# Kernel optimization log

Measured on AMD Instinct MI355X. Metric: run time of the kernel, lower is better.

The kernel has to match this reference:

```python
import jax, jax.numpy as jnp
from jax import lax
import numpy as np

T, B, D, H = 4096, 8, 512, 512


def sru_layer(x, W, b, c0):
    # x: [T,B,D], W: [3H,D], b: [2H], c0: [B,H]
    U = jnp.einsum('tbd,hd->tbh', x, W)          # [T,B,3H] fused projection
    x_tilde, f_pre, r_pre = jnp.split(U, 3, axis=-1)
    f = jax.nn.sigmoid(f_pre + b[:H])            # forget gate [T,B,H]
    r = jax.nn.sigmoid(r_pre + b[H:])            # reset gate  [T,B,H]

    def step(c, inp):
        xt, ft = inp
        c_new = ft * c + (1.0 - ft) * xt         # elementwise recurrence
        return c_new, c_new

    c_last, cs = lax.scan(step, c0, (x_tilde, f))
    h = r * jnp.tanh(cs) + (1.0 - r) * x         # highway connection
    return h, c_last


def setup_inputs() -> dict:
    key = jax.random.key(0)
    k0, k1, k2 = jax.random.split(key, 3)
    scale = 1.0 / np.sqrt(D)
    return {
        'x': jax.random.normal(k0, (T, B, D), dtype=jnp.float32),
        'W0': jax.random.normal(k1, (3 * H, D), dtype=jnp.float32) * scale,
        'b0': jnp.zeros((2 * H,), dtype=jnp.float32),
        'W1': jax.random.normal(k2, (3 * H, H), dtype=jnp.float32) * scale,
        'b1': jnp.zeros((2 * H,), dtype=jnp.float32),
    }


def reference(x, W0, b0, W1, b1):
    c0 = jnp.zeros((x.shape[1], H), dtype=x.dtype)
    h, c = sru_layer(x, W0, b0, c0)
    h, c = sru_layer(h, W1, b1, c0)   # original resets c0 each layer
    return h, c
```

## Files before the change

### kernel.cpp

```cpp
#include <hip/hip_runtime.h>
#include <hip/hip_bf16.h>


#define T_DIM 4096
#define B_DIM 8
#define H_DIM 512
#define M_DIM (T_DIM * B_DIM)
#define N3H 1536
#define K_DIM 512
#define NCHUNK 512
#define CLEN (T_DIM / NCHUNK)
#define NCHAIN (B_DIM * H_DIM)
#define NGRP 32
#define GLEN (NCHUNK / NGRP)

typedef __attribute__((ext_vector_type(8))) short s16x8;
typedef __attribute__((ext_vector_type(4))) float f32x4;
typedef unsigned short ushort_t;
typedef unsigned int uint_t;

__device__ __forceinline__ float bf2f(ushort_t u) {
    return __uint_as_float(((uint_t)u) << 16);
}
__device__ __forceinline__ ushort_t f2bf(float f) {
    uint_t u = __float_as_uint(f);
    u += 0x7FFFu + ((u >> 16) & 1u);
    return (ushort_t)(u >> 16);
}
__device__ __forceinline__ float sigm(float z) {
    return 1.0f / (1.0f + __expf(-z));
}
__device__ __forceinline__ float tanh_fast(float z) {
    float e = __expf(2.0f * z);
    return (e - 1.0f) / (e + 1.0f);
}

#define XF4 (M_DIM * K_DIM / 4)
#define WF4 (N3H * K_DIM / 4)
__global__ void cvt_all(const float* __restrict__ x, const float* __restrict__ w0,
                        const float* __restrict__ w1, ushort_t* __restrict__ xb,
                        ushort_t* __restrict__ w0b, ushort_t* __restrict__ w1b) {
    int i = blockIdx.x * blockDim.x + threadIdx.x;
    const float* src; ushort_t* dst; int idx;
    if (i < XF4) { src = x; dst = xb; idx = i; }
    else if (i < XF4 + WF4) { src = w0; dst = w0b; idx = i - XF4; }
    else if (i < XF4 + 2 * WF4) { src = w1; dst = w1b; idx = i - XF4 - WF4; }
    else return;
    float4 v = reinterpret_cast<const float4*>(src)[idx];
    ushort4 o;
    o.x = f2bf(v.x); o.y = f2bf(v.y); o.z = f2bf(v.z); o.w = f2bf(v.w);
    reinterpret_cast<ushort4*>(dst)[idx] = o;
}

__device__ __forceinline__ s16x8 lds_swz_read(const ushort_t* base, int row, int kb) {
    int byte = (row << 7) + (((kb << 1)) ^ ((row & 7) << 4));
    return *reinterpret_cast<const s16x8*>(reinterpret_cast<const char*>(base) + byte);
}

__global__ __launch_bounds__(512) void gemm_bt256(const ushort_t* __restrict__ A,
                                                  const ushort_t* __restrict__ Bm,
                                                  ushort_t* __restrict__ C,
                                                  int M, int N, int K) {
    __shared__ ushort_t As[2][256 * 64];
    __shared__ ushort_t Bs[2][256 * 64];
    const int ntn = N >> 8;
    const int nwg = gridDim.x;
    const int bid = (int)blockIdx.x;
    const int id = (bid & 7) * (nwg >> 3) + (bid >> 3);
    const int tm = id / ntn, tn = id % ntn;
    const int row0 = tm << 8, col0 = tn << 8;
    const int tid = threadIdx.x;
    const int wv = tid >> 6, lane = tid & 63;
    const int wm = wv >> 2, wn = wv & 3;
    const int l15 = lane & 15;
    const int kgrp = (lane >> 4) << 3;

    f32x4 acc[8][4] = {};

    const int srow_in_wave = lane >> 3;
    const int sslot = lane & 7;

#define STAGE(buf_, t_)                                                                  \
    {                                                                                    \
        const int k0s = (t_) * 64;                                                       \
        _Pragma("unroll")                                                                \
        for (int j = 0; j < 4; ++j) {                                                    \
            const int rl = j * 64 + wv * 8;                                              \
            const int rme = rl + srow_in_wave;                                           \
            const int sl = sslot ^ (rme & 7);             \
            const ushort_t* ga = A + (size_t)(row0 + rme) * K + k0s + (sl << 3);         \
            const ushort_t* gb = Bm + (size_t)(col0 + rme) * K + k0s + (sl << 3);        \
            __builtin_amdgcn_global_load_lds(                                            \
                (const __attribute__((address_space(1))) void*)ga,                       \
                (__attribute__((address_space(3))) void*)&As[buf_][rl * 64], 16, 0, 0);  \
            __builtin_amdgcn_global_load_lds(                                            \
                (const __attribute__((address_space(1))) void*)gb,                       \
                (__attribute__((address_space(3))) void*)&Bs[buf_][rl * 64], 16, 0, 0);  \
        }                                                                                \
    }

    STAGE(0, 0);
    STAGE(1, 1);
    asm volatile("s_waitcnt vmcnt(8)" ::: "memory");
    __builtin_amdgcn_s_barrier();

    const int nkt = K >> 6;
    for (int t = 0; t < nkt; ++t) {
        const int buf = t & 1;
        const ushort_t* Ab = &As[buf][0];
        const ushort_t* Bb = &Bs[buf][0];

        __builtin_amdgcn_s_setprio(1);
        {
            s16x8 af[4][2], bfr[4][2];
#pragma unroll
            for (int j = 0; j < 4; ++j)
#pragma unroll
                for (int kk2 = 0; kk2 < 2; ++kk2)
                    af[j][kk2] = lds_swz_read(Ab, wm * 128 + j * 16 + l15, kk2 * 32 + kgrp);
#pragma unroll
            for (int n = 0; n < 4; ++n)
#pragma unroll
                for (int kk2 = 0; kk2 < 2; ++kk2)
                    bfr[n][kk2] = lds_swz_read(Bb, wn * 64 + n * 16 + l15, kk2 * 32 + kgrp);
#pragma unroll
            for (int j = 0; j < 4; ++j)
#pragma unroll
                for (int n = 0; n < 4; ++n)
#pragma unroll
                    for (int kk2 = 0; kk2 < 2; ++kk2)
                        acc[j][n] = __builtin_amdgcn_mfma_f32_16x16x32_bf16(af[j][kk2], bfr[n][kk2], acc[j][n], 0, 0, 0);
#pragma unroll
            for (int j = 0; j < 4; ++j)
#pragma unroll
                for (int kk2 = 0; kk2 < 2; ++kk2)
                    af[j][kk2] = lds_swz_read(Ab, wm * 128 + (4 + j) * 16 + l15, kk2 * 32 + kgrp);
#pragma unroll
            for (int j = 0; j < 4; ++j)
#pragma unroll
                for (int n = 0; n < 4; ++n)
#pragma unroll
                    for (int kk2 = 0; kk2 < 2; ++kk2)
                        acc[4 + j][n] = __builtin_amdgcn_mfma_f32_16x16x32_bf16(af[j][kk2], bfr[n][kk2], acc[4 + j][n], 0, 0, 0);
        }
        __builtin_amdgcn_s_setprio(0);
        __builtin_amdgcn_s_barrier();

        if (t + 2 < nkt) STAGE(buf, t + 2);
        if (t + 1 < nkt) {
            if (t + 2 < nkt) asm volatile("s_waitcnt vmcnt(8)" ::: "memory");
            else             asm volatile("s_waitcnt vmcnt(0)" ::: "memory");
            __builtin_amdgcn_s_barrier();
        }
    }
#undef STAGE

    const int crow = (lane >> 4) << 2;
#pragma unroll
    for (int m = 0; m < 8; ++m)
#pragma unroll
        for (int n = 0; n < 4; ++n)
#pragma unroll
            for (int v = 0; v < 4; ++v)
                C[(size_t)(row0 + wm * 128 + m * 16 + crow + v) * N + (col0 + wn * 64 + n * 16 + l15)] =
                    f2bf(acc[m][n][v]);
}

__global__ void scan_summary(const ushort_t* __restrict__ U, const float* __restrict__ bias,
                             float* __restrict__ Sa, float* __restrict__ Sb) {
    const int b = blockIdx.x / NCHUNK;
    const int chunk = blockIdx.x % NCHUNK;
    const int h = threadIdx.x << 2;
    float fb[4];
#pragma unroll
    for (int j = 0; j < 4; ++j) fb[j] = bias[h + j];
    float Aa[4] = {1.f, 1.f, 1.f, 1.f};
    float Bb[4] = {0.f, 0.f, 0.f, 0.f};
    const ushort_t* rp = U + ((size_t)(chunk * CLEN) * B_DIM + b) * N3H + h;
    ushort4 xt = *reinterpret_cast<const ushort4*>(rp);
    ushort4 fp = *reinterpret_cast<const ushort4*>(rp + H_DIM);
#pragma unroll
    for (int s = 0; s < CLEN; ++s) {
        ushort4 xt_n, fp_n;
        if (s + 1 < CLEN) {
            rp += (size_t)B_DIM * N3H;
            xt_n = *reinterpret_cast<const ushort4*>(rp);
            fp_n = *reinterpret_cast<const ushort4*>(rp + H_DIM);
        }
        float xs[4] = {bf2f(xt.x), bf2f(xt.y), bf2f(xt.z), bf2f(xt.w)};
        float fs[4] = {bf2f(fp.x), bf2f(fp.y), bf2f(fp.z), bf2f(fp.w)};
#pragma unroll
        for (int j = 0; j < 4; ++j) {
            float f = sigm(fs[j] + fb[j]);
            Aa[j] *= f;
            Bb[j] = f * Bb[j] + (1.f - f) * xs[j];
        }
        xt = xt_n; fp = fp_n;
    }
    const int cb = chunk * NCHAIN + b * H_DIM + h;
#pragma unroll
    for (int j = 0; j < 4; ++j) { Sa[cb + j] = Aa[j]; Sb[cb + j] = Bb[j]; }
}

__global__ void scan_fixup1(float* Sa, float* Sb, float* __restrict__ Ga, float* __restrict__ Gb) {
    const int idx = blockIdx.x * blockDim.x + threadIdx.x;
    const int chain = idx & (NCHAIN - 1);
    const int g = idx >> 12;
    float A = 1.f, B = 0.f;
#pragma unroll
    for (int i = 0; i < GLEN; ++i) {
        const size_t off = (size_t)(g * GLEN + i) * NCHAIN + chain;
        float a = Sa[off], b = Sb[off];
        Sa[off] = A; Sb[off] = B;
        B = a * B + b;
        A = a * A;
    }
    Ga[g * NCHAIN + chain] = A;
    Gb[g * NCHAIN + chain] = B;
}

__global__ void scan_fixup2(const float* __restrict__ Ga, const float* __restrict__ Gb,
                            float* __restrict__ Eg, float* __restrict__ clast) {
    const int chain = blockIdx.x * blockDim.x + threadIdx.x;
    float c = 0.f;
#pragma unroll
    for (int g = 0; g < NGRP; ++g) {
        Eg[g * NCHAIN + chain] = c;
        c = Ga[g * NCHAIN + chain] * c + Gb[g * NCHAIN + chain];
    }
    if (clast) clast[chain] = c;
}

template <bool IN_BF16, bool OUT_BF16>
__global__ void scan_apply(const ushort_t* __restrict__ U, const float* __restrict__ bias,
                           const float* __restrict__ Sa, const float* __restrict__ Sb,
                           const float* __restrict__ Eg,
                           const void* __restrict__ xin, void* __restrict__ hout) {
    const int b = blockIdx.x / NCHUNK;
    const int chunk = blockIdx.x % NCHUNK;
    const int h = threadIdx.x << 2;
    const int cb = chunk * NCHAIN + b * H_DIM + h;
    const int eb = (chunk >> 4) * NCHAIN + b * H_DIM + h;
    float cc[4], fb[4], rb[4];
    float4 la = *reinterpret_cast<const float4*>(&Sa[cb]);
    float4 lb = *reinterpret_cast<const float4*>(&Sb[cb]);
    float4 eg = *reinterpret_cast<const float4*>(&Eg[eb]);
    cc[0] = lb.x + la.x * eg.x; cc[1] = lb.y + la.y * eg.y;
    cc[2] = lb.z + la.z * eg.z; cc[3] = lb.w + la.w * eg.w;
#pragma unroll
    for (int j = 0; j < 4; ++j) {
        fb[j] = bias[h + j];
        rb[j] = bias[H_DIM + h + j];
    }
    size_t row = (size_t)(chunk * CLEN) * B_DIM + b;
    const ushort_t* rp = U + row * N3H + h;
    size_t xoff = row * H_DIM + h;

    ushort4 xt = *reinterpret_cast<const ushort4*>(rp);
    ushort4 fp = *reinterpret_cast<const ushort4*>(rp + H_DIM);
    ushort4 rr = *reinterpret_cast<const ushort4*>(rp + 2 * H_DIM);
    float xv[4];
    if (IN_BF16) {
        ushort4 xi = *reinterpret_cast<const ushort4*>((const ushort_t*)xin + xoff);
        xv[0] = bf2f(xi.x); xv[1] = bf2f(xi.y); xv[2] = bf2f(xi.z); xv[3] = bf2f(xi.w);
    } else {
        float4 xi = *reinterpret_cast<const float4*>((const float*)xin + xoff);
        xv[0] = xi.x; xv[1] = xi.y; xv[2] = xi.z; xv[3] = xi.w;
    }

#pragma unroll
    for (int s = 0; s < CLEN; ++s) {
        ushort4 xt_n, fp_n, rr_n;
        float xv_n[4];
        if (s + 1 < CLEN) {
            rp += (size_t)B_DIM * N3H;
            xt_n = *reinterpret_cast<const ushort4*>(rp);
            fp_n = *reinterpret_cast<const ushort4*>(rp + H_DIM);
            rr_n = *reinterpret_cast<const ushort4*>(rp + 2 * H_DIM);
            size_t xo2 = xoff + (size_t)B_DIM * H_DIM;
            if (IN_BF16) {
                ushort4 xi = *reinterpret_cast<const ushort4*>((const ushort_t*)xin + xo2);
                xv_n[0] = bf2f(xi.x); xv_n[1] = bf2f(xi.y); xv_n[2] = bf2f(xi.z); xv_n[3] = bf2f(xi.w);
            } else {
                float4 xi = *reinterpret_cast<const float4*>((const float*)xin + xo2);
                xv_n[0] = xi.x; xv_n[1] = xi.y; xv_n[2] = xi.z; xv_n[3] = xi.w;
            }
        }
        float xts[4] = {bf2f(xt.x), bf2f(xt.y), bf2f(xt.z), bf2f(xt.w)};
        float fps[4] = {bf2f(fp.x), bf2f(fp.y), bf2f(fp.z), bf2f(fp.w)};
        float rps[4] = {bf2f(rr.x), bf2f(rr.y), bf2f(rr.z), bf2f(rr.w)};
        float hv[4];
#pragma unroll
        for (int j = 0; j < 4; ++j) {
            float f = sigm(fps[j] + fb[j]);
            cc[j] = f * cc[j] + (1.f - f) * xts[j];
            float r = sigm(rps[j] + rb[j]);
            hv[j] = r * tanh_fast(cc[j]) + (1.f - r) * xv[j];
        }
        if (OUT_BF16) {
            ushort4 o;
            o.x = f2bf(hv[0]); o.y = f2bf(hv[1]); o.z = f2bf(hv[2]); o.w = f2bf(hv[3]);
            *reinterpret_cast<ushort4*>((ushort_t*)hout + xoff) = o;
        } else {
            float4 o;
            o.x = hv[0]; o.y = hv[1]; o.z = hv[2]; o.w = hv[3];
            *reinterpret_cast<float4*>((float*)hout + xoff) = o;
        }
        xoff += (size_t)B_DIM * H_DIM;
        xt = xt_n; fp = fp_n; rr = rr_n;
        xv[0] = xv_n[0]; xv[1] = xv_n[1]; xv[2] = xv_n[2]; xv[3] = xv_n[3];
    }
}

extern "C" void kernel_launch(void* const* d_in, const int* in_sizes, int n_in,
                              void* d_out, int out_size, void* d_ws, size_t ws_size,
                              hipStream_t stream) {
    (void)in_sizes; (void)n_in; (void)out_size; (void)ws_size;
    const float* x  = (const float*)d_in[0];
    const float* W0 = (const float*)d_in[1];
    const float* b0 = (const float*)d_in[2];
    const float* W1 = (const float*)d_in[3];
    const float* b1 = (const float*)d_in[4];
    float* out = (float*)d_out;

    char* ws = (char*)d_ws;
    ushort_t* xb  = (ushort_t*)(ws);
    float*    Sa  = (float*)(ws);
    float*    Sb  = (float*)(ws + 8388608);
    float*    Ga  = (float*)(ws + 16777216);
    float*    Gb  = (float*)(ws + 17301504);
    float*    Eg  = (float*)(ws + 17825792);
    ushort_t* h1  = (ushort_t*)(ws + 33554432);
    ushort_t* W0b = (ushort_t*)(ws + 67108864);
    ushort_t* W1b = (ushort_t*)(ws + 68681728);
    ushort_t* U   = (ushort_t*)(ws + 70254592);

    const int cvt_total = XF4 + 2 * WF4;
    cvt_all<<<(cvt_total + 255) / 256, 256, 0, stream>>>(x, W0, W1, xb, W0b, W1b);

    const int gemm_grid = (M_DIM / 256) * (N3H / 256);
    const int scan_grid = B_DIM * NCHUNK;

    gemm_bt256<<<gemm_grid, 512, 0, stream>>>(xb, W0b, U, M_DIM, N3H, K_DIM);
    scan_summary<<<scan_grid, 128, 0, stream>>>(U, b0, Sa, Sb);
    scan_fixup1<<<NGRP * NCHAIN / 256, 256, 0, stream>>>(Sa, Sb, Ga, Gb);
    scan_fixup2<<<NCHAIN / 256, 256, 0, stream>>>(Ga, Gb, Eg, nullptr);
    scan_apply<false, true><<<scan_grid, 128, 0, stream>>>(U, b0, Sa, Sb, Eg, (const void*)x, (void*)h1);

    gemm_bt256<<<gemm_grid, 512, 0, stream>>>(h1, W1b, U, M_DIM, N3H, K_DIM);
    scan_summary<<<scan_grid, 128, 0, stream>>>(U, b1, Sa, Sb);
    scan_fixup1<<<NGRP * NCHAIN / 256, 256, 0, stream>>>(Sa, Sb, Ga, Gb);
    scan_fixup2<<<NCHAIN / 256, 256, 0, stream>>>(Ga, Gb, Eg, out + (size_t)M_DIM * H_DIM);
    scan_apply<true, false><<<scan_grid, 128, 0, stream>>>(U, b1, Sa, Sb, Eg, (const void*)h1, (void*)out);
}
```

Before: 285.3 us.

## Load GEMM B operand directly into registers and halve LDS footprint

The GEMM no longer stages the weight (B) tile through LDS. Each wave loads its B fragments straight from global memory into double-buffered registers one k-tile ahead, while A stays double-buffered in LDS. Halving LDS use and setting launch bounds to 2 blocks per CU is meant to raise occupancy and cut LDS traffic, and the K loop is fully unrolled with compile-time dimensions. The cost is more register pressure and uncoalesced per-wave global loads of B, which now rely on cache reuse across waves.

```diff
diff --git a/kernel.cpp b/kernel.cpp
--- a/kernel.cpp
+++ b/kernel.cpp
@@ -8,6 +8,7 @@
 #define M_DIM (T_DIM * B_DIM)
 #define N3H 1536
 #define K_DIM 512
+#define NKT (K_DIM / 64)
 #define NCHUNK 512
 #define CLEN (T_DIM / NCHUNK)
 #define NCHAIN (B_DIM * H_DIM)
@@ -57,13 +58,11 @@
     return *reinterpret_cast<const s16x8*>(reinterpret_cast<const char*>(base) + byte);
 }
 
-__global__ __launch_bounds__(512) void gemm_bt256(const ushort_t* __restrict__ A,
-                                                  const ushort_t* __restrict__ Bm,
-                                                  ushort_t* __restrict__ C,
-                                                  int M, int N, int K) {
+__global__ __launch_bounds__(512, 2) void gemm_bt256(const ushort_t* __restrict__ A,
+                                                     const ushort_t* __restrict__ Bm,
+                                                     ushort_t* __restrict__ C) {
     __shared__ ushort_t As[2][256 * 64];
-    __shared__ ushort_t Bs[2][256 * 64];
-    const int ntn = N >> 8;
+    const int ntn = N3H >> 8;
     const int nwg = gridDim.x;
     const int bid = (int)blockIdx.x;
     const int id = (bid & 7) * (nwg >> 3) + (bid >> 3);
@@ -80,7 +79,21 @@
     const int srow_in_wave = lane >> 3;
     const int sslot = lane & 7;
 
-#define STAGE(buf_, t_)                                                                  \
+    const ushort_t* Bg = Bm + (size_t)(col0 + wn * 64 + l15) * K_DIM + kgrp;
+
+    s16x8 bE[8], bO[8];
+
+#define LOADB(bank_, t_)                                                                 \
+    {                                                                                    \
+        _Pragma("unroll")                                                                \
+        for (int n = 0; n < 4; ++n)                                                      \
+            _Pragma("unroll")                                                            \
+            for (int kk2 = 0; kk2 < 2; ++kk2)                                            \
+                bank_[n * 2 + kk2] = *reinterpret_cast<const s16x8*>(                    \
+                    Bg + (size_t)(n * 16) * K_DIM + (t_) * 64 + kk2 * 32);               \
+    }
+
+#define STAGE_A(buf_, t_)                                                                \
     {                                                                                    \
         const int k0s = (t_) * 64;                                                       \
         _Pragma("unroll")                                                                \
@@ -88,72 +101,77 @@
             const int rl = j * 64 + wv * 8;                                              \
             const int rme = rl + srow_in_wave;                                           \
             const int sl = sslot ^ (rme & 7);             \
-            const ushort_t* ga = A + (size_t)(row0 + rme) * K + k0s + (sl << 3);         \
-            const ushort_t* gb = Bm + (size_t)(col0 + rme) * K + k0s + (sl << 3);        \
+            const ushort_t* ga = A + (size_t)(row0 + rme) * K_DIM + k0s + (sl << 3);     \
             __builtin_amdgcn_global_load_lds(                                            \
                 (const __attribute__((address_space(1))) void*)ga,                       \
                 (__attribute__((address_space(3))) void*)&As[buf_][rl * 64], 16, 0, 0);  \
-            __builtin_amdgcn_global_load_lds(                                            \
-                (const __attribute__((address_space(1))) void*)gb,                       \
-                (__attribute__((address_space(3))) void*)&Bs[buf_][rl * 64], 16, 0, 0);  \
         }                                                                                \
     }
 
-    STAGE(0, 0);
-    STAGE(1, 1);
-    asm volatile("s_waitcnt vmcnt(8)" ::: "memory");
+#define COMPUTE(Ab_, bk_)                                                                \
+    {                                                                                    \
+        s16x8 af[4][2];                                                                  \
+        _Pragma("unroll")                                                                \
+        for (int m = 0; m < 4; ++m)                                                      \
+            _Pragma("unroll")                                                            \
+            for (int kk2 = 0; kk2 < 2; ++kk2)                                            \
+                af[m][kk2] = lds_swz_read(Ab_, wm * 128 + m * 16 + l15, kk2 * 32 + kgrp);\
+        _Pragma("unroll")                                                                \
+        for (int m = 0; m < 4; ++m)                                                      \
+            _Pragma("unroll")                                                            \
+            for (int n = 0; n < 4; ++n)                                                  \
+                _Pragma("unroll")                                                        \
+                for (int kk2 = 0; kk2 < 2; ++kk2)                                        \
+                    acc[m][n] = __builtin_amdgcn_mfma_f32_16x16x32_bf16(                 \
+                        af[m][kk2], bk_[n * 2 + kk2], acc[m][n], 0, 0, 0);               \
+        _Pragma("unroll")                                                                \
+        for (int m = 0; m < 4; ++m)                                                      \
+            _Pragma("unroll")                                                            \
+            for (int kk2 = 0; kk2 < 2; ++kk2)                                            \
+                af[m][kk2] = lds_swz_read(Ab_, wm * 128 + (4 + m) * 16 + l15,            \
+                                          kk2 * 32 + kgrp);                              \
+        _Pragma("unroll")                                                                \
+        for (int m = 0; m < 4; ++m)                                                      \
+            _Pragma("unroll")                                                            \
+            for (int n = 0; n < 4; ++n)                                                  \
+                _Pragma("unroll")                                                        \
+                for (int kk2 = 0; kk2 < 2; ++kk2)                                        \
+                    acc[4 + m][n] = __builtin_amdgcn_mfma_f32_16x16x32_bf16(             \
+                        af[m][kk2], bk_[n * 2 + kk2], acc[4 + m][n], 0, 0, 0);           \
+    }
+
+#define TILE_BODY(t_, buf_, bkC_, bkN_)                                                  \
+    {                                                                                    \
+        if ((t_) + 1 < NKT) LOADB(bkN_, (t_) + 1);                                       \
+        __builtin_amdgcn_s_setprio(1);                                                   \
+        COMPUTE(&As[buf_][0], bkC_);                                                     \
+        __builtin_amdgcn_s_setprio(0);                                                   \
+        __builtin_amdgcn_s_barrier();               \
+        if ((t_) + 2 < NKT) {                                                            \
+            STAGE_A(buf_, (t_) + 2);                                                     \
+            asm volatile("s_waitcnt vmcnt(12)" ::: "memory");         \
+            __builtin_amdgcn_s_barrier();                                                \
+        } else if ((t_) + 1 < NKT) {                                                     \
+            asm volatile("s_waitcnt vmcnt(8)" ::: "memory");          \
+            __builtin_amdgcn_s_barrier();                                                \
+        }                                                                                \
+    }
+
+    STAGE_A(0, 0);
+    STAGE_A(1, 1);
+    LOADB(bE, 0);
+    asm volatile("s_waitcnt vmcnt(12)" ::: "memory");
     __builtin_amdgcn_s_barrier();
 
-    const int nkt = K >> 6;
-    for (int t = 0; t < nkt; ++t) {
-        const int buf = t & 1;
-        const ushort_t* Ab = &As[buf][0];
-        const ushort_t* Bb = &Bs[buf][0];
-
-        __builtin_amdgcn_s_setprio(1);
-        {
-            s16x8 af[4][2], bfr[4][2];
-#pragma unroll
-            for (int j = 0; j < 4; ++j)
-#pragma unroll
-                for (int kk2 = 0; kk2 < 2; ++kk2)
-                    af[j][kk2] = lds_swz_read(Ab, wm * 128 + j * 16 + l15, kk2 * 32 + kgrp);
-#pragma unroll
-            for (int n = 0; n < 4; ++n)
-#pragma unroll
-                for (int kk2 = 0; kk2 < 2; ++kk2)
-                    bfr[n][kk2] = lds_swz_read(Bb, wn * 64 + n * 16 + l15, kk2 * 32 + kgrp);
-#pragma unroll
-            for (int j = 0; j < 4; ++j)
-#pragma unroll
-                for (int n = 0; n < 4; ++n)
-#pragma unroll
-                    for (int kk2 = 0; kk2 < 2; ++kk2)
-                        acc[j][n] = __builtin_amdgcn_mfma_f32_16x16x32_bf16(af[j][kk2], bfr[n][kk2], acc[j][n], 0, 0, 0);
-#pragma unroll
-            for (int j = 0; j < 4; ++j)
-#pragma unroll
-                for (int kk2 = 0; kk2 < 2; ++kk2)
-                    af[j][kk2] = lds_swz_read(Ab, wm * 128 + (4 + j) * 16 + l15, kk2 * 32 + kgrp);
-#pragma unroll
-            for (int j = 0; j < 4; ++j)
-#pragma unroll
-                for (int n = 0; n < 4; ++n)
-#pragma unroll
-                    for (int kk2 = 0; kk2 < 2; ++kk2)
-                        acc[4 + j][n] = __builtin_amdgcn_mfma_f32_16x16x32_bf16(af[j][kk2], bfr[n][kk2], acc[4 + j][n], 0, 0, 0);
-        }
-        __builtin_amdgcn_s_setprio(0);
-        __builtin_amdgcn_s_barrier();
-
-        if (t + 2 < nkt) STAGE(buf, t + 2);
-        if (t + 1 < nkt) {
-            if (t + 2 < nkt) asm volatile("s_waitcnt vmcnt(8)" ::: "memory");
-            else             asm volatile("s_waitcnt vmcnt(0)" ::: "memory");
-            __builtin_amdgcn_s_barrier();
-        }
-    }
-#undef STAGE
+#pragma unroll
+    for (int tp = 0; tp < NKT / 2; ++tp) {
+        TILE_BODY(tp * 2, 0, bE, bO);
+        TILE_BODY(tp * 2 + 1, 1, bO, bE);
+    }
+#undef TILE_BODY
+#undef COMPUTE
+#undef STAGE_A
+#undef LOADB
 
     const int crow = (lane >> 4) << 2;
 #pragma unroll
@@ -162,7 +180,7 @@
         for (int n = 0; n < 4; ++n)
 #pragma unroll
             for (int v = 0; v < 4; ++v)
-                C[(size_t)(row0 + wm * 128 + m * 16 + crow + v) * N + (col0 + wn * 64 + n * 16 + l15)] =
+                C[(size_t)(row0 + wm * 128 + m * 16 + crow + v) * N3H + (col0 + wn * 64 + n * 16 + l15)] =
                     f2bf(acc[m][n][v]);
 }
 
@@ -341,13 +359,13 @@
     const int gemm_grid = (M_DIM / 256) * (N3H / 256);
     const int scan_grid = B_DIM * NCHUNK;
 
-    gemm_bt256<<<gemm_grid, 512, 0, stream>>>(xb, W0b, U, M_DIM, N3H, K_DIM);
+    gemm_bt256<<<gemm_grid, 512, 0, stream>>>(xb, W0b, U);
     scan_summary<<<scan_grid, 128, 0, stream>>>(U, b0, Sa, Sb);
     scan_fixup1<<<NGRP * NCHAIN / 256, 256, 0, stream>>>(Sa, Sb, Ga, Gb);
     scan_fixup2<<<NCHAIN / 256, 256, 0, stream>>>(Ga, Gb, Eg, nullptr);
     scan_apply<false, true><<<scan_grid, 128, 0, stream>>>(U, b0, Sa, Sb, Eg, (const void*)x, (void*)h1);
 
-    gemm_bt256<<<gemm_grid, 512, 0, stream>>>(h1, W1b, U, M_DIM, N3H, K_DIM);
+    gemm_bt256<<<gemm_grid, 512, 0, stream>>>(h1, W1b, U);
     scan_summary<<<scan_grid, 128, 0, stream>>>(U, b1, Sa, Sb);
     scan_fixup1<<<NGRP * NCHAIN / 256, 256, 0, stream>>>(Sa, Sb, Ga, Gb);
     scan_fixup2<<<NCHAIN / 256, 256, 0, stream>>>(Ga, Gb, Eg, out + (size_t)M_DIM * H_DIM);
```

Result: slower. 316.1 us (+10.8%).

## Restructure GEMM main loop into 8-wave half-tile staged ping-pong schedule

Applied to the files above, without the earlier changes.

The bf16 GEMM's K-loop is rebuilt so the A and B tiles are each split into two 128-row halves. Global-to-LDS loads for those halves are issued one half at a time between four MFMA quadrants per K step, separated by barriers and priority toggles, and the loop over the compile-time K count is fully unrolled. The aim is finer interleaving of memory traffic with matrix-core work and hiding load latency across the 8 waves. K/N become compile-time constants and launch bounds request 2 blocks per SM. The cost is more barriers per iteration, and occupancy is likely still capped by the 128KB of LDS per block.

```diff
diff --git a/kernel.cpp b/kernel.cpp
--- a/kernel.cpp
+++ b/kernel.cpp
@@ -8,6 +8,7 @@
 #define M_DIM (T_DIM * B_DIM)
 #define N3H 1536
 #define K_DIM 512
+#define NKT (K_DIM / 64)
 #define NCHUNK 512
 #define CLEN (T_DIM / NCHUNK)
 #define NCHAIN (B_DIM * H_DIM)
@@ -57,13 +58,12 @@
     return *reinterpret_cast<const s16x8*>(reinterpret_cast<const char*>(base) + byte);
 }
 
-__global__ __launch_bounds__(512) void gemm_bt256(const ushort_t* __restrict__ A,
-                                                  const ushort_t* __restrict__ Bm,
-                                                  ushort_t* __restrict__ C,
-                                                  int M, int N, int K) {
-    __shared__ ushort_t As[2][256 * 64];
-    __shared__ ushort_t Bs[2][256 * 64];
-    const int ntn = N >> 8;
+__global__ __launch_bounds__(512, 2) void gemm_bt256(const ushort_t* __restrict__ A,
+                                                     const ushort_t* __restrict__ Bm,
+                                                     ushort_t* __restrict__ C) {
+    __shared__ ushort_t As[2][2][128 * 64];
+    __shared__ ushort_t Bs[2][2][128 * 64];
+    const int ntn = N3H >> 8;
     const int nwg = gridDim.x;
     const int bid = (int)blockIdx.x;
     const int id = (bid & 7) * (nwg >> 3) + (bid >> 3);
@@ -77,83 +77,106 @@
 
     f32x4 acc[8][4] = {};
 
-    const int srow_in_wave = lane >> 3;
-    const int sslot = lane & 7;
-
-#define STAGE(buf_, t_)                                                                  \
+    const int srw = lane >> 3;
+    const int ssl = lane & 7;
+
+#define STAGE_H(ARR, GP, BASE0, hh, t_, d_)                                              \
     {                                                                                    \
-        const int k0s = (t_) * 64;                                                       \
         _Pragma("unroll")                                                                \
-        for (int j = 0; j < 4; ++j) {                                                    \
-            const int rl = j * 64 + wv * 8;                                              \
-            const int rme = rl + srow_in_wave;                                           \
-            const int sl = sslot ^ (rme & 7);             \
-            const ushort_t* ga = A + (size_t)(row0 + rme) * K + k0s + (sl << 3);         \
-            const ushort_t* gb = Bm + (size_t)(col0 + rme) * K + k0s + (sl << 3);        \
+        for (int j = 0; j < 2; ++j) {                                                    \
+            const int rl = j * 64 + wv * 8 + srw;                                        \
+            const int sl = ssl ^ (rl & 7);                                               \
+            const ushort_t* gp_ = (GP) + (size_t)((BASE0) + (hh) * 128 + rl) * K_DIM     \
+                                  + (t_) * 64 + (sl << 3);                               \
             __builtin_amdgcn_global_load_lds(                                            \
-                (const __attribute__((address_space(1))) void*)ga,                       \
-                (__attribute__((address_space(3))) void*)&As[buf_][rl * 64], 16, 0, 0);  \
-            __builtin_amdgcn_global_load_lds(                                            \
-                (const __attribute__((address_space(1))) void*)gb,                       \
-                (__attribute__((address_space(3))) void*)&Bs[buf_][rl * 64], 16, 0, 0);  \
+                (const __attribute__((address_space(1))) void*)gp_,                      \
+                (__attribute__((address_space(3))) void*)&ARR[d_][hh][(j * 64 + wv * 8) * 64], \
+                16, 0, 0);                                                               \
         }                                                                                \
     }
 
-    STAGE(0, 0);
-    STAGE(1, 1);
-    asm volatile("s_waitcnt vmcnt(8)" ::: "memory");
+#define LDA_HALF(mbase_)                                                                 \
+    _Pragma("unroll")                                                                    \
+    for (int m = 0; m < 4; ++m)                                                          \
+        _Pragma("unroll")                                                                \
+        for (int kk = 0; kk < 2; ++kk)                                                   \
+            af[m][kk] = lds_swz_read(&As[buf][wm][0], (mbase_ + m) * 16 + l15,           \
+                                     kk * 32 + kgrp);
+
+#define LDB_PAIR(nbase_)                                                                 \
+    _Pragma("unroll")                                                                    \
+    for (int n = 0; n < 2; ++n)                                                          \
+        _Pragma("unroll")                                                                \
+        for (int kk = 0; kk < 2; ++kk)                                                   \
+            bfr[(nbase_) + n][kk] = lds_swz_read(&Bs[buf][wn >> 1][0],                   \
+                (wn & 1) * 64 + ((nbase_) + n) * 16 + l15, kk * 32 + kgrp);
+
+#define MFMA_Q(mbase_, nbase_)                                                           \
+    _Pragma("unroll")                                                                    \
+    for (int m = 0; m < 4; ++m)                                                          \
+        _Pragma("unroll")                                                                \
+        for (int n = 0; n < 2; ++n)                                                      \
+            _Pragma("unroll")                                                            \
+            for (int kk = 0; kk < 2; ++kk)                                               \
+                acc[(mbase_) + m][(nbase_) + n] = __builtin_amdgcn_mfma_f32_16x16x32_bf16( \
+                    af[m][kk], bfr[(nbase_) + n][kk], acc[(mbase_) + m][(nbase_) + n],   \
+                    0, 0, 0);
+
+    STAGE_H(Bs, Bm, col0, 0, 0, 0);
+    STAGE_H(As, A, row0, 0, 0, 0);
+    STAGE_H(Bs, Bm, col0, 1, 0, 0);
+    STAGE_H(As, A, row0, 1, 0, 0);
+    STAGE_H(Bs, Bm, col0, 0, 1, 1);
+    STAGE_H(As, A, row0, 0, 1, 1);
+    asm volatile("s_waitcnt vmcnt(4)" ::: "memory");
     __builtin_amdgcn_s_barrier();
 
-    const int nkt = K >> 6;
-    for (int t = 0; t < nkt; ++t) {
-        const int buf = t & 1;
-        const ushort_t* Ab = &As[buf][0];
-        const ushort_t* Bb = &Bs[buf][0];
-
+#pragma unroll
+    for (int u = 0; u < NKT; ++u) {
+        const int buf = u & 1;
+        s16x8 af[4][2], bfr[4][2];
+
+        LDA_HALF(0);
+        LDB_PAIR(0);
+        if (u + 1 < NKT) { STAGE_H(Bs, Bm, col0, 1, u + 1, buf ^ 1); }
+        __builtin_amdgcn_s_barrier();
+        asm volatile("s_waitcnt lgkmcnt(0)" ::: "memory");
         __builtin_amdgcn_s_setprio(1);
-        {
-            s16x8 af[4][2], bfr[4][2];
-#pragma unroll
-            for (int j = 0; j < 4; ++j)
-#pragma unroll
-                for (int kk2 = 0; kk2 < 2; ++kk2)
-                    af[j][kk2] = lds_swz_read(Ab, wm * 128 + j * 16 + l15, kk2 * 32 + kgrp);
-#pragma unroll
-            for (int n = 0; n < 4; ++n)
-#pragma unroll
-                for (int kk2 = 0; kk2 < 2; ++kk2)
-                    bfr[n][kk2] = lds_swz_read(Bb, wn * 64 + n * 16 + l15, kk2 * 32 + kgrp);
-#pragma unroll
-            for (int j = 0; j < 4; ++j)
-#pragma unroll
-                for (int n = 0; n < 4; ++n)
-#pragma unroll
-                    for (int kk2 = 0; kk2 < 2; ++kk2)
-                        acc[j][n] = __builtin_amdgcn_mfma_f32_16x16x32_bf16(af[j][kk2], bfr[n][kk2], acc[j][n], 0, 0, 0);
-#pragma unroll
-            for (int j = 0; j < 4; ++j)
-#pragma unroll
-                for (int kk2 = 0; kk2 < 2; ++kk2)
-                    af[j][kk2] = lds_swz_read(Ab, wm * 128 + (4 + j) * 16 + l15, kk2 * 32 + kgrp);
-#pragma unroll
-            for (int j = 0; j < 4; ++j)
-#pragma unroll
-                for (int n = 0; n < 4; ++n)
-#pragma unroll
-                    for (int kk2 = 0; kk2 < 2; ++kk2)
-                        acc[4 + j][n] = __builtin_amdgcn_mfma_f32_16x16x32_bf16(af[j][kk2], bfr[n][kk2], acc[4 + j][n], 0, 0, 0);
-        }
+        MFMA_Q(0, 0);
         __builtin_amdgcn_s_setprio(0);
         __builtin_amdgcn_s_barrier();
 
-        if (t + 2 < nkt) STAGE(buf, t + 2);
-        if (t + 1 < nkt) {
-            if (t + 2 < nkt) asm volatile("s_waitcnt vmcnt(8)" ::: "memory");
-            else             asm volatile("s_waitcnt vmcnt(0)" ::: "memory");
-            __builtin_amdgcn_s_barrier();
-        }
-    }
-#undef STAGE
+        LDB_PAIR(2);
+        if (u + 1 < NKT) { STAGE_H(As, A, row0, 1, u + 1, buf ^ 1); }
+        __builtin_amdgcn_s_barrier();
+        asm volatile("s_waitcnt lgkmcnt(0)" ::: "memory");
+        __builtin_amdgcn_s_setprio(1);
+        MFMA_Q(0, 2);
+        __builtin_amdgcn_s_setprio(0);
+        __builtin_amdgcn_s_barrier();
+
+        LDA_HALF(4);
+        if (u + 2 < NKT) { STAGE_H(Bs, Bm, col0, 0, u + 2, buf); }
+        __builtin_amdgcn_s_barrier();
+        asm volatile("s_waitcnt lgkmcnt(0)" ::: "memory");
+        __builtin_amdgcn_s_setprio(1);
+        MFMA_Q(4, 0);
+        __builtin_amdgcn_s_setprio(0);
+        __builtin_amdgcn_s_barrier();
+
+        if (u + 2 < NKT) { STAGE_H(As, A, row0, 0, u + 2, buf); }
+        __builtin_amdgcn_s_barrier();
+        __builtin_amdgcn_s_setprio(1);
+        MFMA_Q(4, 2);
+        __builtin_amdgcn_s_setprio(0);
+        if (u + 2 < NKT)      { asm volatile("s_waitcnt vmcnt(4)" ::: "memory"); }
+        else if (u + 1 < NKT) { asm volatile("s_waitcnt vmcnt(0)" ::: "memory"); }
+        __builtin_amdgcn_s_barrier();
+    }
+#undef MFMA_Q
+#undef LDB_PAIR
+#undef LDA_HALF
+#undef STAGE_H
 
     const int crow = (lane >> 4) << 2;
 #pragma unroll
@@ -162,7 +185,7 @@
         for (int n = 0; n < 4; ++n)
 #pragma unroll
             for (int v = 0; v < 4; ++v)
-                C[(size_t)(row0 + wm * 128 + m * 16 + crow + v) * N + (col0 + wn * 64 + n * 16 + l15)] =
+                C[(size_t)(row0 + wm * 128 + m * 16 + crow + v) * N3H + (col0 + wn * 64 + n * 16 + l15)] =
                     f2bf(acc[m][n][v]);
 }
 
@@ -341,13 +364,13 @@
     const int gemm_grid = (M_DIM / 256) * (N3H / 256);
     const int scan_grid = B_DIM * NCHUNK;
 
-    gemm_bt256<<<gemm_grid, 512, 0, stream>>>(xb, W0b, U, M_DIM, N3H, K_DIM);
+    gemm_bt256<<<gemm_grid, 512, 0, stream>>>(xb, W0b, U);
     scan_summary<<<scan_grid, 128, 0, stream>>>(U, b0, Sa, Sb);
     scan_fixup1<<<NGRP * NCHAIN / 256, 256, 0, stream>>>(Sa, Sb, Ga, Gb);
     scan_fixup2<<<NCHAIN / 256, 256, 0, stream>>>(Ga, Gb, Eg, nullptr);
     scan_apply<false, true><<<scan_grid, 128, 0, stream>>>(U, b0, Sa, Sb, Eg, (const void*)x, (void*)h1);
 
-    gemm_bt256<<<gemm_grid, 512, 0, stream>>>(h1, W1b, U, M_DIM, N3H, K_DIM);
+    gemm_bt256<<<gemm_grid, 512, 0, stream>>>(h1, W1b, U);
     scan_summary<<<scan_grid, 128, 0, stream>>>(U, b1, Sa, Sb);
     scan_fixup1<<<NGRP * NCHAIN / 256, 256, 0, stream>>>(Sa, Sb, Ga, Gb);
     scan_fixup2<<<NCHAIN / 256, 256, 0, stream>>>(Ga, Gb, Eg, out + (size_t)M_DIM * H_DIM);
```

Result: no change. 283.8 us (-0.5%).
